# Kernel tuning notes

Measured on AMD Instinct MI355X. Metric: run time of the kernel, lower is better.

## Reference

```python
import jax, jax.numpy as jnp
import numpy as np

B, T, D, H = 4, 2048, 1024, 16
HD = D // H  # head_size = 64


def setup_inputs() -> dict:
    key = jax.random.key(0)
    ks = jax.random.split(key, 6)
    s = 0.02
    x = jax.random.normal(ks[0], (B, T, D), dtype=jnp.float32)
    # per-head unfused projections, stacked over heads: [H, D, HD]
    Wq = jax.random.normal(ks[1], (H, D, HD), dtype=jnp.float32) * s
    Wk = jax.random.normal(ks[2], (H, D, HD), dtype=jnp.float32) * s
    Wv = jax.random.normal(ks[3], (H, D, HD), dtype=jnp.float32) * s
    # output projection, torch Linear layout [out, in]
    Wo = jax.random.normal(ks[4], (D, D), dtype=jnp.float32) * s
    bo = jax.random.normal(ks[5], (D,), dtype=jnp.float32) * s
    return {"x": x, "Wq": Wq, "Wk": Wk, "Wv": Wv, "Wo": Wo, "bo": bo}


def reference(x, Wq, Wk, Wv, Wo, bo):
    b, t, d = x.shape
    hd = Wq.shape[-1]
    q = jnp.einsum('btd,hdk->bhtk', x, Wq)
    k = jnp.einsum('btd,hdk->bhtk', x, Wk)
    v = jnp.einsum('btd,hdk->bhtk', x, Wv)
    scores = jnp.einsum('bhtk,bhsk->bhts', q, k) / jnp.sqrt(jnp.float32(hd))
    mask = jnp.tril(jnp.ones((t, t), dtype=bool))  # causal
    scores = jnp.where(mask, scores, jnp.float32(-jnp.inf))
    p = jax.nn.softmax(scores, axis=-1)
    o = jnp.einsum('bhts,bhsk->bhtk', p, v)
    o = o.transpose(0, 2, 1, 3).reshape(b, t, d)  # concat heads
    return o @ Wo.T + bo
```

## Files before the change

### kernel.cpp

```cpp
#include <hip/hip_runtime.h>
#include <hip/hip_bf16.h>
#include <stdint.h>

#define B_   4
#define T_   2048
#define D_   1024
#define H_   16
#define HD_  64
#define MROWS (B_*T_)
#define NQKV  3072
#define NST  (T_/64)

typedef __attribute__((ext_vector_type(8))) short  short8;
typedef __attribute__((ext_vector_type(4))) short  bf16x4;
typedef __attribute__((ext_vector_type(4))) float  floatx4;

#define QSCALE 0.1803368801111244f

__device__ inline void async_copy16(const __hip_bfloat16* g, __hip_bfloat16* l) {
  __builtin_amdgcn_global_load_lds(
      (const __attribute__((address_space(1))) void*)g,
      (__attribute__((address_space(3))) void*)l, 16, 0, 0);
}

__device__ inline floatx4 mfma16(bf16x4 a, bf16x4 b, floatx4 c) {
#if __has_builtin(__builtin_amdgcn_mfma_f32_16x16x16bf16_1k)
  return __builtin_amdgcn_mfma_f32_16x16x16bf16_1k(a, b, c, 0, 0, 0);
#elif __has_builtin(__builtin_amdgcn_mfma_f32_16x16x16_bf16)
  return __builtin_amdgcn_mfma_f32_16x16x16_bf16(a, b, c, 0, 0, 0);
#else
  short8 a8 = (short8){a[0], a[1], a[2], a[3], 0, 0, 0, 0};
  short8 b8 = (short8){b[0], b[1], b[2], b[3], 0, 0, 0, 0};
  return __builtin_amdgcn_mfma_f32_16x16x32_bf16(a8, b8, c, 0, 0, 0);
#endif
}

__global__ void prep(const float* __restrict__ x, const float* __restrict__ Wo,
                     const float* __restrict__ Wq, const float* __restrict__ Wk,
                     const float* __restrict__ Wv,
                     __hip_bfloat16* __restrict__ xb, __hip_bfloat16* __restrict__ wob,
                     __hip_bfloat16* __restrict__ wqkv) {
  __shared__ __hip_bfloat16 tile[64][65];
  const int bid = (int)blockIdx.x;
  const int t = threadIdx.x;
  if (bid < 8192) {
    int i = (bid * 256 + t) * 4;
    float4 v = *(const float4*)(x + i);
    xb[i + 0] = __float2bfloat16(v.x);
    xb[i + 1] = __float2bfloat16(v.y);
    xb[i + 2] = __float2bfloat16(v.z);
    xb[i + 3] = __float2bfloat16(v.w);
  } else if (bid < 9216) {
    int i = ((bid - 8192) * 256 + t) * 4;
    float4 v = *(const float4*)(Wo + i);
    wob[i + 0] = __float2bfloat16(v.x);
    wob[i + 1] = __float2bfloat16(v.y);
    wob[i + 2] = __float2bfloat16(v.z);
    wob[i + 3] = __float2bfloat16(v.w);
  } else {
    int idx = bid - 9216;
    const int d0 = (idx & 15) * 64;
    const int wh = idx >> 4;
    const int which = wh >> 4, h = wh & 15;
    const float* W = (which == 0) ? Wq : ((which == 1) ? Wk : Wv);
    const float* base = W + (size_t)h * D_ * HD_;
#pragma unroll
    for (int i = 0; i < 16; i++) {
      int e = i * 256 + t;
      int dr = e >> 6, hd = e & 63;
      tile[dr][hd] = __float2bfloat16(base[(size_t)(d0 + dr) * HD_ + hd]);
    }
    __syncthreads();
#pragma unroll
    for (int i = 0; i < 16; i++) {
      int e = i * 256 + t;
      int hd = e >> 6, dr = e & 63;
      wqkv[(size_t)(which * 1024 + h * 64 + hd) * D_ + d0 + dr] = tile[dr][hd];
    }
  }
}

__global__ void repack_kv(const __hip_bfloat16* __restrict__ qkv,
                          __hip_bfloat16* __restrict__ kpack, __hip_bfloat16* __restrict__ vpack) {
  __shared__ __hip_bfloat16 Ks[64][72];
  __shared__ __hip_bfloat16 Vs[64][72];
  const int tid = threadIdx.x;
  const int st = blockIdx.x, bh = blockIdx.y;
  const int b = bh >> 4, h = bh & 15;
#pragma unroll
  for (int p = 0; p < 2; p++) {
    int c = p * 256 + tid;
    int row = c >> 3, col8 = c & 7;
    const __hip_bfloat16* src = qkv + (size_t)(b * T_ + st * 64 + row) * NQKV + h * HD_ + col8 * 8;
    *(uint4*)&Ks[row][col8 * 8] = *(const uint4*)(src + 1024);
    *(uint4*)&Vs[row][col8 * 8] = *(const uint4*)(src + 2048);
  }
  __syncthreads();
  const size_t base = ((size_t)bh * NST + st) * 8 * 512;
#pragma unroll
  for (int p = 0; p < 2; p++) {
    int pair = p * 256 + tid;
    int c = pair >> 6, l = pair & 63;
    int lq = l & 15, q = l >> 4;
    int ni = c >> 1, half = c & 1;
    short8 v = *(const short8*)&Ks[ni * 16 + lq][half * 32 + q * 8];
    *(short8*)(kpack + base + (size_t)c * 512 + l * 8) = v;
  }
#pragma unroll
  for (int p = 0; p < 2; p++) {
    int pair = p * 256 + tid;
    int c = pair >> 6, l = pair & 63;
    int lq = l & 15, q = l >> 4;
    int m = c >> 2, nt = c & 3;
    __hip_bfloat16 tmp[8];
#pragma unroll
    for (int half = 0; half < 2; half++)
#pragma unroll
      for (int j = 0; j < 4; j++)
        tmp[half * 4 + j] = Vs[(2 * m + half) * 16 + q * 4 + j][nt * 16 + lq];
    *(short8*)(vpack + base + (size_t)c * 512 + l * 8) = *(short8*)tmp;
  }
}


__device__ inline void stage16k(const __hip_bfloat16* __restrict__ grow0, int K,
                                short* ldst, int tid) {
#pragma unroll
  for (int l = 0; l < 2; ++l) {
    int c = l * 512 + tid;
    int r = c >> 3;
    int sw = (c & 7) ^ (r & 7);
    async_copy16(grow0 + (size_t)r * K + sw * 8, (__hip_bfloat16*)(ldst + c * 8));
  }
}

__device__ inline short8 fragld2(const short* base, int r, int slot) {
  return *(const short8*)(base + r * 64 + (((slot) ^ (r & 7)) << 3));
}

__launch_bounds__(512, 2)
__global__ void gemmk(const __hip_bfloat16* __restrict__ A, const __hip_bfloat16* __restrict__ Bt,
                      __hip_bfloat16* __restrict__ Cb, int M, int N, int K, float qscale) {
  __shared__ short LDS[49152];
  const int tid = threadIdx.x;
  const int lane = tid & 63, wid = tid >> 6;
  const int lq = lane & 15, quad = lane >> 4;
  const int wr = wid >> 2, wc = wid & 3;

  const int lin = (int)blockIdx.x;
  const int s = (lin & 7) * 96 + (lin >> 3);
  const int m0 = (s / 12) * 128, n0 = (s % 12) * 256;

  const int NT = K >> 6;

  floatx4 acc[4][4];
#pragma unroll
  for (int i = 0; i < 4; i++)
#pragma unroll
    for (int j = 0; j < 4; j++) acc[i][j] = (floatx4){0.f, 0.f, 0.f, 0.f};

  {
    short* b0s = LDS;
    stage16k(A  + (size_t)m0 * K,          K, b0s,         tid);
    stage16k(Bt + (size_t)n0 * K,          K, b0s + 8192,  tid);
    stage16k(Bt + (size_t)(n0 + 128) * K,  K, b0s + 16384, tid);
    short* b1s = LDS + 24576;
    stage16k(A  + (size_t)m0 * K + 64,     K, b1s,         tid);
    stage16k(Bt + (size_t)n0 * K + 64,     K, b1s + 8192,  tid);
  }
  asm volatile("s_waitcnt vmcnt(4)" ::: "memory");
  __builtin_amdgcn_s_barrier();

#pragma unroll 1
  for (int t = 0; t < NT; ++t) {
    short* buf = LDS + (t & 1) * 24576;
    short* nbuf = LDS + ((t & 1) ^ 1) * 24576;
    const int kc1 = (t + 1) << 6, kc2 = (t + 2) << 6;

    short8 a[4][2], b[2][2];
#pragma unroll
    for (int mi = 0; mi < 4; ++mi)
#pragma unroll
      for (int kk = 0; kk < 2; ++kk)
        a[mi][kk] = fragld2(buf, wr * 64 + mi * 16 + lq, kk * 4 + quad);
#pragma unroll
    for (int f = 0; f < 2; ++f)
#pragma unroll
      for (int kk = 0; kk < 2; ++kk)
        b[f][kk] = fragld2(buf + 8192, wc * 32 + f * 16 + lq, kk * 4 + quad);
    if (t + 1 < NT)
      stage16k(Bt + (size_t)(n0 + 128) * K + kc1, K, nbuf + 16384, tid);
    __builtin_amdgcn_s_barrier();
    __builtin_amdgcn_s_setprio(1);
#pragma unroll
    for (int kk = 0; kk < 2; ++kk)
#pragma unroll
      for (int mi = 0; mi < 4; ++mi)
#pragma unroll
        for (int f = 0; f < 2; ++f)
          acc[mi][f] = __builtin_amdgcn_mfma_f32_16x16x32_bf16(a[mi][kk], b[f][kk], acc[mi][f], 0, 0, 0);
    __builtin_amdgcn_s_setprio(0);
    __builtin_amdgcn_s_barrier();

    short8 b2[2][2];
#pragma unroll
    for (int f = 0; f < 2; ++f)
#pragma unroll
      for (int kk = 0; kk < 2; ++kk)
        b2[f][kk] = fragld2(buf + 8192, 128 + wc * 32 + f * 16 + lq, kk * 4 + quad);
    if (t + 2 < NT) {
      stage16k(A  + (size_t)m0 * K + kc2, K, buf,        tid);
      stage16k(Bt + (size_t)n0 * K + kc2, K, buf + 8192, tid);
    }
    __builtin_amdgcn_s_barrier();
    __builtin_amdgcn_s_setprio(1);
#pragma unroll
    for (int kk = 0; kk < 2; ++kk)
#pragma unroll
      for (int mi = 0; mi < 4; ++mi)
#pragma unroll
        for (int f = 0; f < 2; ++f)
          acc[mi][2 + f] = __builtin_amdgcn_mfma_f32_16x16x32_bf16(a[mi][kk], b2[f][kk], acc[mi][2 + f], 0, 0, 0);
    __builtin_amdgcn_s_setprio(0);
    if (t + 2 < NT)      { asm volatile("s_waitcnt vmcnt(4)" ::: "memory"); }
    else if (t + 1 < NT) { asm volatile("s_waitcnt vmcnt(0)" ::: "memory"); }
    __builtin_amdgcn_s_barrier();
  }

#pragma unroll
  for (int mi = 0; mi < 4; ++mi) {
#pragma unroll
    for (int nh = 0; nh < 2; ++nh)
#pragma unroll
      for (int f = 0; f < 2; ++f) {
        int col = n0 + nh * 128 + wc * 32 + f * 16 + lq;
        float sc = (col < 1024) ? qscale : 1.0f;
#pragma unroll
        for (int r = 0; r < 4; ++r) {
          int row = m0 + wr * 64 + mi * 16 + quad * 4 + r;
          Cb[(size_t)row * N + col] = __float2bfloat16(acc[mi][nh * 2 + f][r] * sc);
        }
      }
  }
}

template <int EPI>
__launch_bounds__(256, 2)
__global__ void gemm_bt(const __hip_bfloat16* __restrict__ A, const __hip_bfloat16* __restrict__ Bt,
                        __hip_bfloat16* __restrict__ Cb, float* __restrict__ Cf,
                        const float* __restrict__ bias, int M, int N, int K, float qscale) {
  __shared__ __hip_bfloat16 As[128 * 32];
  __shared__ __hip_bfloat16 Bs[128 * 32];
  const int tid = threadIdx.x;
  const int w = tid >> 6, lane = tid & 63;
  const int lq = lane & 15, quad = lane >> 4;
  const int wr = w >> 1, wc = w & 1;
  const int m0 = blockIdx.x * 128, n0 = blockIdx.y * 128;

  floatx4 acc[4][4];
#pragma unroll
  for (int i = 0; i < 4; i++)
#pragma unroll
    for (int j = 0; j < 4; j++) acc[i][j] = (floatx4){0.f, 0.f, 0.f, 0.f};

  for (int k0 = 0; k0 < K; k0 += 32) {
    __syncthreads();
#pragma unroll
    for (int ph = 0; ph < 2; ++ph) {
      int c = ph * 256 + tid;
      int row = c >> 2, col8 = c & 3;
      async_copy16(A + (size_t)(m0 + row) * K + k0 + col8 * 8, As + c * 8);
      async_copy16(Bt + (size_t)(n0 + row) * K + k0 + col8 * 8, Bs + c * 8);
    }
    __syncthreads();
    short8 af[4], bf[4];
#pragma unroll
    for (int mi = 0; mi < 4; mi++)
      af[mi] = *(const short8*)(As + (wr * 64 + mi * 16 + lq) * 32 + quad * 8);
#pragma unroll
    for (int ni = 0; ni < 4; ni++)
      bf[ni] = *(const short8*)(Bs + (wc * 64 + ni * 16 + lq) * 32 + quad * 8);
#pragma unroll
    for (int mi = 0; mi < 4; mi++)
#pragma unroll
      for (int ni = 0; ni < 4; ni++)
        acc[mi][ni] = __builtin_amdgcn_mfma_f32_16x16x32_bf16(af[mi], bf[ni], acc[mi][ni], 0, 0, 0);
  }

#pragma unroll
  for (int mi = 0; mi < 4; mi++) {
#pragma unroll
    for (int ni = 0; ni < 4; ni++) {
      int col = n0 + wc * 64 + ni * 16 + lq;
      if (EPI == 0) {
        float s = (col < 1024) ? qscale : 1.0f;
#pragma unroll
        for (int r = 0; r < 4; r++) {
          int row = m0 + wr * 64 + mi * 16 + quad * 4 + r;
          Cb[(size_t)row * N + col] = __float2bfloat16(acc[mi][ni][r] * s);
        }
      } else {
        float bv = bias[col];
#pragma unroll
        for (int r = 0; r < 4; r++) {
          int row = m0 + wr * 64 + mi * 16 + quad * 4 + r;
          Cf[(size_t)row * N + col] = acc[mi][ni][r] + bv;
        }
      }
    }
  }
}

__launch_bounds__(256, 2)
__global__ void attn(const __hip_bfloat16* __restrict__ qkv,
                     const __hip_bfloat16* __restrict__ kpack,
                     const __hip_bfloat16* __restrict__ vpack,
                     __hip_bfloat16* __restrict__ obuf) {
  __shared__ __hip_bfloat16 KVs[2][8192];
  const int tid = threadIdx.x;
  const int w = tid >> 6, lane = tid & 63;
  const int lq = lane & 15, quad = lane >> 4;

  const int bh = (int)blockIdx.x;
  const int a  = (int)blockIdx.y;
  const int b = bh >> 4, h = bh & 15;

  const __hip_bfloat16* kbase = kpack + ((size_t)bh * NST) * 4096;
  const __hip_bfloat16* vbase = vpack + ((size_t)bh * NST) * 4096;

#pragma unroll 1
  for (int seg = 0; seg < 2; ++seg) {
    const int tbase = seg ? (NST - 2 - 2 * a) : (2 * a);
    const int qt = tbase + (w >> 1);
    const int rbase = (w & 1) * 32;

    short8 qf[2][2];
#pragma unroll
    for (int bi = 0; bi < 2; bi++) {
      const __hip_bfloat16* qp =
          qkv + ((size_t)(b * T_ + qt * 64 + rbase + bi * 16 + lq)) * NQKV + h * HD_;
      qf[bi][0] = *(const short8*)(qp + quad * 8);
      qf[bi][1] = *(const short8*)(qp + 32 + quad * 8);
    }

    floatx4 Oacc[2][4];
#pragma unroll
    for (int bi = 0; bi < 2; bi++)
#pragma unroll
      for (int i = 0; i < 4; i++) Oacc[bi][i] = (floatx4){0.f, 0.f, 0.f, 0.f};
    float lrow[2] = {0.f, 0.f};

    const int itTop = tbase + 1;

#pragma unroll
    for (int j = 0; j < 2; ++j) {
      int c = j * 256 + tid;
      async_copy16(kbase + (size_t)c * 8, &KVs[0][0] + c * 8);
      async_copy16(vbase + (size_t)c * 8, &KVs[0][4096] + c * 8);
    }
    __syncthreads();

#pragma unroll 1
    for (int it = 0; it <= itTop; ++it) {
      const int cur = it & 1;
      if (it < itTop) {
        const __hip_bfloat16* kn = kbase + (size_t)(it + 1) * 4096;
        const __hip_bfloat16* vn = vbase + (size_t)(it + 1) * 4096;
#pragma unroll
        for (int j = 0; j < 2; ++j) {
          int c = j * 256 + tid;
          async_copy16(kn + (size_t)c * 8, &KVs[cur ^ 1][0] + c * 8);
          async_copy16(vn + (size_t)c * 8, &KVs[cur ^ 1][4096] + c * 8);
        }
      }
      if (it <= qt) {
        const __hip_bfloat16* Kb = &KVs[cur][0] + lane * 8;
        const __hip_bfloat16* Vb = &KVs[cur][4096] + lane * 8;
        short8 kf[4], kg[4];
#pragma unroll
        for (int ni = 0; ni < 4; ni++) {
          kf[ni] = *(const short8*)(Kb + (size_t)(ni * 2 + 0) * 512);
          kg[ni] = *(const short8*)(Kb + (size_t)(ni * 2 + 1) * 512);
        }
        short8 vfr[8];
#pragma unroll
        for (int c = 0; c < 8; c++) vfr[c] = *(const short8*)(Vb + (size_t)c * 512);

        floatx4 Sc[2][4];
        __builtin_amdgcn_s_setprio(1);
#pragma unroll
        for (int bi = 0; bi < 2; bi++)
#pragma unroll
          for (int ni = 0; ni < 4; ni++) {
            floatx4 c0 = (floatx4){0.f, 0.f, 0.f, 0.f};
            c0 = __builtin_amdgcn_mfma_f32_16x16x32_bf16(kf[ni], qf[bi][0], c0, 0, 0, 0);
            c0 = __builtin_amdgcn_mfma_f32_16x16x32_bf16(kg[ni], qf[bi][1], c0, 0, 0, 0);
            Sc[bi][ni] = c0;
          }
        __builtin_amdgcn_s_setprio(0);

        if (it == qt) {
#pragma unroll
          for (int bi = 0; bi < 2; bi++) {
            int lrow_idx = rbase + bi * 16 + lq;
#pragma unroll
            for (int ni = 0; ni < 4; ni++)
#pragma unroll
              for (int r = 0; r < 4; r++) {
                int s_loc = ni * 16 + quad * 4 + r;
                if (s_loc > lrow_idx) Sc[bi][ni][r] = -__builtin_inff();
              }
          }
        }

        bf16x4 pf[2][4];
#pragma unroll
        for (int bi = 0; bi < 2; bi++)
#pragma unroll
          for (int c = 0; c < 4; c++) {
            __hip_bfloat16 pb[4];
#pragma unroll
            for (int r = 0; r < 4; r++) {
              float p = __builtin_amdgcn_exp2f(Sc[bi][c][r]);
              lrow[bi] += p;
              pb[r] = __float2bfloat16(p);
            }
            pf[bi][c] = *(bf16x4*)pb;
          }

        __builtin_amdgcn_s_setprio(1);
#pragma unroll
        for (int m = 0; m < 2; m++)
#pragma unroll
          for (int nt = 0; nt < 4; nt++) {
            short8 v8 = vfr[m * 4 + nt];
            bf16x4 vlo = (bf16x4){v8[0], v8[1], v8[2], v8[3]};
            bf16x4 vhi = (bf16x4){v8[4], v8[5], v8[6], v8[7]};
#pragma unroll
            for (int bi = 0; bi < 2; bi++) {
              Oacc[bi][nt] = mfma16(pf[bi][2 * m + 0], vlo, Oacc[bi][nt]);
              Oacc[bi][nt] = mfma16(pf[bi][2 * m + 1], vhi, Oacc[bi][nt]);
            }
          }
        __builtin_amdgcn_s_setprio(0);
      }
      __syncthreads();
    }

#pragma unroll
    for (int bi = 0; bi < 2; bi++) {
      float ps = lrow[bi];
      ps += __shfl_xor(ps, 16);
      ps += __shfl_xor(ps, 32);
      float inv = 1.0f / ps;
#pragma unroll
      for (int r = 0; r < 4; r++) {
        float invr = __shfl(inv, quad * 4 + r);
        int t = qt * 64 + rbase + bi * 16 + quad * 4 + r;
#pragma unroll
        for (int nt = 0; nt < 4; nt++)
          obuf[(size_t)(b * T_ + t) * D_ + h * HD_ + nt * 16 + lq] =
              __float2bfloat16(Oacc[bi][nt][r] * invr);
      }
    }
  }
}


extern "C" void kernel_launch(void* const* d_in, const int* in_sizes, int n_in,
                              void* d_out, int out_size, void* d_ws, size_t ws_size,
                              hipStream_t stream) {
  const float* x  = (const float*)d_in[0];
  const float* Wq = (const float*)d_in[1];
  const float* Wk = (const float*)d_in[2];
  const float* Wv = (const float*)d_in[3];
  const float* Wo = (const float*)d_in[4];
  const float* bo = (const float*)d_in[5];
  float* out = (float*)d_out;

  char* ws = (char*)d_ws;
  __hip_bfloat16* xb    = (__hip_bfloat16*)(ws);
  __hip_bfloat16* obuf  = (__hip_bfloat16*)(ws);
  __hip_bfloat16* wqkv  = (__hip_bfloat16*)(ws + ((size_t)16 << 20));
  __hip_bfloat16* wob   = (__hip_bfloat16*)(ws + ((size_t)22 << 20));
  __hip_bfloat16* qkv   = (__hip_bfloat16*)(ws + ((size_t)24 << 20));
  __hip_bfloat16* kpack = (__hip_bfloat16*)(ws + ((size_t)72 << 20));
  __hip_bfloat16* vpack = (__hip_bfloat16*)(ws + ((size_t)88 << 20));

  prep<<<9984, 256, 0, stream>>>(x, Wo, Wq, Wk, Wv, xb, wob, wqkv);

  gemmk<<<768, 512, 0, stream>>>(xb, wqkv, qkv, MROWS, NQKV, D_, QSCALE);

  repack_kv<<<dim3(NST, B_ * H_), 256, 0, stream>>>(qkv, kpack, vpack);

  attn<<<dim3(B_ * H_, 8), 256, 0, stream>>>(qkv, kpack, vpack, obuf);

  gemm_bt<1><<<dim3(MROWS / 128, D_ / 128), 256, 0, stream>>>(
      obuf, wob, nullptr, out, bo, MROWS, D_, D_, 1.0f);
}
```

Measured before the change: 257.2 us.

## Widen QKV GEMM tiles to 128x384 with a simple double-buffered pipeline

Replaces the 128x256 QKV projection GEMM with a 128x384 tile, where each wave holds 4x6 accumulator fragments. This cuts the grid from 768 to 512 blocks, which divides evenly over the CUs, and gives each block more reuse of the staged A rows. The hand-tuned split-phase pipeline with explicit vmcnt waits becomes a plain two-stage double buffer synchronized with __syncthreads. In exchange, LDS per block grows to 128KB and register pressure rises from the 24 accumulators, and the simpler synchronization may expose more load latency.

```diff
diff --git a/kernel.cpp b/kernel.cpp
--- a/kernel.cpp
+++ b/kernel.cpp
@@ -139,108 +139,90 @@
 }
 
 __launch_bounds__(512, 2)
-__global__ void gemmk(const __hip_bfloat16* __restrict__ A, const __hip_bfloat16* __restrict__ Bt,
+__global__ void gemmq(const __hip_bfloat16* __restrict__ A, const __hip_bfloat16* __restrict__ Bt,
                       __hip_bfloat16* __restrict__ Cb, int M, int N, int K, float qscale) {
-  __shared__ short LDS[49152];
+  __shared__ short LDS[2][32768];
   const int tid = threadIdx.x;
   const int lane = tid & 63, wid = tid >> 6;
   const int lq = lane & 15, quad = lane >> 4;
   const int wr = wid >> 2, wc = wid & 3;
 
   const int lin = (int)blockIdx.x;
-  const int s = (lin & 7) * 96 + (lin >> 3);
-  const int m0 = (s / 12) * 128, n0 = (s % 12) * 256;
+  const int s = (lin & 7) * 64 + (lin >> 3);
+  const int m0 = (s & 63) * 128, n0 = (s >> 6) * 384;
 
   const int NT = K >> 6;
 
-  floatx4 acc[4][4];
+  floatx4 acc[4][6];
 #pragma unroll
   for (int i = 0; i < 4; i++)
 #pragma unroll
-    for (int j = 0; j < 4; j++) acc[i][j] = (floatx4){0.f, 0.f, 0.f, 0.f};
+    for (int j = 0; j < 6; j++) acc[i][j] = (floatx4){0.f, 0.f, 0.f, 0.f};
 
   {
-    short* b0s = LDS;
-    stage16k(A  + (size_t)m0 * K,          K, b0s,         tid);
-    stage16k(Bt + (size_t)n0 * K,          K, b0s + 8192,  tid);
-    stage16k(Bt + (size_t)(n0 + 128) * K,  K, b0s + 16384, tid);
-    short* b1s = LDS + 24576;
-    stage16k(A  + (size_t)m0 * K + 64,     K, b1s,         tid);
-    stage16k(Bt + (size_t)n0 * K + 64,     K, b1s + 8192,  tid);
-  }
-  asm volatile("s_waitcnt vmcnt(4)" ::: "memory");
-  __builtin_amdgcn_s_barrier();
+    short* b0 = &LDS[0][0];
+    stage16k(A + (size_t)m0 * K, K, b0, tid);
+#pragma unroll
+    for (int j = 0; j < 3; ++j)
+      stage16k(Bt + (size_t)(n0 + 128 * j) * K, K, b0 + 8192 + 8192 * j, tid);
+  }
 
 #pragma unroll 1
   for (int t = 0; t < NT; ++t) {
-    short* buf = LDS + (t & 1) * 24576;
-    short* nbuf = LDS + ((t & 1) ^ 1) * 24576;
-    const int kc1 = (t + 1) << 6, kc2 = (t + 2) << 6;
-
-    short8 a[4][2], b[2][2];
+    __syncthreads();
+    const short* buf = &LDS[t & 1][0];
+    short* nb = &LDS[(t & 1) ^ 1][0];
+    const int kc = (t + 1) << 6;
+
+    short8 a0[4], b0[6];
 #pragma unroll
     for (int mi = 0; mi < 4; ++mi)
-#pragma unroll
-      for (int kk = 0; kk < 2; ++kk)
-        a[mi][kk] = fragld2(buf, wr * 64 + mi * 16 + lq, kk * 4 + quad);
-#pragma unroll
-    for (int f = 0; f < 2; ++f)
-#pragma unroll
-      for (int kk = 0; kk < 2; ++kk)
-        b[f][kk] = fragld2(buf + 8192, wc * 32 + f * 16 + lq, kk * 4 + quad);
-    if (t + 1 < NT)
-      stage16k(Bt + (size_t)(n0 + 128) * K + kc1, K, nbuf + 16384, tid);
-    __builtin_amdgcn_s_barrier();
+      a0[mi] = fragld2(buf, wr * 64 + mi * 16 + lq, quad);
+#pragma unroll
+    for (int ni = 0; ni < 6; ++ni)
+      b0[ni] = fragld2(buf + 8192, wc * 96 + ni * 16 + lq, quad);
+    if (t + 1 < NT) {
+      stage16k(A + (size_t)m0 * K + kc, K, nb, tid);
+#pragma unroll
+      for (int j = 0; j < 3; ++j)
+        stage16k(Bt + (size_t)(n0 + 128 * j) * K + kc, K, nb + 8192 + 8192 * j, tid);
+    }
     __builtin_amdgcn_s_setprio(1);
 #pragma unroll
-    for (int kk = 0; kk < 2; ++kk)
-#pragma unroll
-      for (int mi = 0; mi < 4; ++mi)
-#pragma unroll
-        for (int f = 0; f < 2; ++f)
-          acc[mi][f] = __builtin_amdgcn_mfma_f32_16x16x32_bf16(a[mi][kk], b[f][kk], acc[mi][f], 0, 0, 0);
+    for (int mi = 0; mi < 4; ++mi)
+#pragma unroll
+      for (int ni = 0; ni < 6; ++ni)
+        acc[mi][ni] = __builtin_amdgcn_mfma_f32_16x16x32_bf16(a0[mi], b0[ni], acc[mi][ni], 0, 0, 0);
     __builtin_amdgcn_s_setprio(0);
-    __builtin_amdgcn_s_barrier();
-
-    short8 b2[2][2];
-#pragma unroll
-    for (int f = 0; f < 2; ++f)
-#pragma unroll
-      for (int kk = 0; kk < 2; ++kk)
-        b2[f][kk] = fragld2(buf + 8192, 128 + wc * 32 + f * 16 + lq, kk * 4 + quad);
-    if (t + 2 < NT) {
-      stage16k(A  + (size_t)m0 * K + kc2, K, buf,        tid);
-      stage16k(Bt + (size_t)n0 * K + kc2, K, buf + 8192, tid);
-    }
-    __builtin_amdgcn_s_barrier();
+
+    short8 a1[4], b1[6];
+#pragma unroll
+    for (int mi = 0; mi < 4; ++mi)
+      a1[mi] = fragld2(buf, wr * 64 + mi * 16 + lq, 4 + quad);
+#pragma unroll
+    for (int ni = 0; ni < 6; ++ni)
+      b1[ni] = fragld2(buf + 8192, wc * 96 + ni * 16 + lq, 4 + quad);
     __builtin_amdgcn_s_setprio(1);
 #pragma unroll
-    for (int kk = 0; kk < 2; ++kk)
-#pragma unroll
-      for (int mi = 0; mi < 4; ++mi)
-#pragma unroll
-        for (int f = 0; f < 2; ++f)
-          acc[mi][2 + f] = __builtin_amdgcn_mfma_f32_16x16x32_bf16(a[mi][kk], b2[f][kk], acc[mi][2 + f], 0, 0, 0);
+    for (int mi = 0; mi < 4; ++mi)
+#pragma unroll
+      for (int ni = 0; ni < 6; ++ni)
+        acc[mi][ni] = __builtin_amdgcn_mfma_f32_16x16x32_bf16(a1[mi], b1[ni], acc[mi][ni], 0, 0, 0);
     __builtin_amdgcn_s_setprio(0);
-    if (t + 2 < NT)      { asm volatile("s_waitcnt vmcnt(4)" ::: "memory"); }
-    else if (t + 1 < NT) { asm volatile("s_waitcnt vmcnt(0)" ::: "memory"); }
-    __builtin_amdgcn_s_barrier();
   }
 
 #pragma unroll
   for (int mi = 0; mi < 4; ++mi) {
 #pragma unroll
-    for (int nh = 0; nh < 2; ++nh)
-#pragma unroll
-      for (int f = 0; f < 2; ++f) {
-        int col = n0 + nh * 128 + wc * 32 + f * 16 + lq;
-        float sc = (col < 1024) ? qscale : 1.0f;
-#pragma unroll
-        for (int r = 0; r < 4; ++r) {
-          int row = m0 + wr * 64 + mi * 16 + quad * 4 + r;
-          Cb[(size_t)row * N + col] = __float2bfloat16(acc[mi][nh * 2 + f][r] * sc);
-        }
+    for (int ni = 0; ni < 6; ++ni) {
+      int col = n0 + wc * 96 + ni * 16 + lq;
+      float sc = (col < 1024) ? qscale : 1.0f;
+#pragma unroll
+      for (int r = 0; r < 4; ++r) {
+        int row = m0 + wr * 64 + mi * 16 + quad * 4 + r;
+        Cb[(size_t)row * N + col] = __float2bfloat16(acc[mi][ni][r] * sc);
       }
+    }
   }
 }
 
@@ -489,7 +471,7 @@
 
   prep<<<9984, 256, 0, stream>>>(x, Wo, Wq, Wk, Wv, xb, wob, wqkv);
 
-  gemmk<<<768, 512, 0, stream>>>(xb, wqkv, qkv, MROWS, NQKV, D_, QSCALE);
+  gemmq<<<512, 512, 0, stream>>>(xb, wqkv, qkv, MROWS, NQKV, D_, QSCALE);
 
   repack_kv<<<dim3(NST, B_ * H_), 256, 0, stream>>>(qkv, kpack, vpack);
 
```

Result: faster. 237.4 us (-7.7%).
